# Kernel optimization log

Measured on AMD Instinct MI355X. Metric: run time of the kernel, lower is better.

## Reference

```python
import jax, jax.numpy as jnp
import numpy as np
from math import sqrt

D_MODEL, D_COND, N_HEADS = 512, 768, 8
B, H, W, L_COND = 8, 64, 64, 256


def setup_inputs() -> dict:
    key = jax.random.key(0)
    ks = jax.random.split(key, 7)
    return {
        "image": jax.random.normal(ks[0], (B, D_MODEL, H, W), jnp.float32),
        "cond": jax.random.normal(ks[1], (B, L_COND, D_COND), jnp.float32),
        "attention_mask": jnp.zeros((B, H * W, L_COND), jnp.float32),
        "Wq": jax.random.normal(ks[2], (D_MODEL, D_MODEL), jnp.float32) * 0.02,
        "Wk": jax.random.normal(ks[3], (D_MODEL, D_COND), jnp.float32) * 0.02,
        "Wv": jax.random.normal(ks[4], (D_MODEL, D_COND), jnp.float32) * 0.02,
        "Wo": jax.random.normal(ks[5], (D_MODEL, D_MODEL), jnp.float32) * 0.02,
        "bo": jnp.zeros((D_MODEL,), jnp.float32),
    }


def reference(image, cond, attention_mask, Wq, Wk, Wv, Wo, bo):
    b, d, h, w = image.shape
    L = h * w
    n = N_HEADS
    dh = d // n
    scale = sqrt(dh)
    # b d h w -> b l d
    x = image.reshape(b, d, L).transpose(0, 2, 1)
    # projections (torch Linear: y = x @ W.T), split heads: b l (n dh) -> b n l dh
    q = (x @ Wq.T).reshape(b, L, n, dh).transpose(0, 2, 1, 3)
    k = (cond @ Wk.T).reshape(b, -1, n, dh).transpose(0, 2, 1, 3)
    v = (cond @ Wv.T).reshape(b, -1, n, dh).transpose(0, 2, 1, 3)
    attn = jnp.einsum("bnqd,bnkd->bnqk", q, k) / scale
    attn = attn + attention_mask[:, None]  # b 1 L L_cond
    p = jax.nn.softmax(attn, axis=-1)
    o = jnp.einsum("bnqk,bnkd->bnqd", p, v)  # b n L dh
    # b n (h w) dh -> b (n dh) h w
    o = o.transpose(0, 1, 3, 2).reshape(b, d, h, w)
    # 1x1 conv == per-pixel linear over channels
    out = jnp.einsum("oc,bchw->bohw", Wo, o) + bo[None, :, None, None]
    return out
```

## Files before the change

### kernel.cpp

```cpp
#include <hip/hip_runtime.h>

typedef __bf16 bf16x8 __attribute__((ext_vector_type(8)));
typedef float f32x4 __attribute__((ext_vector_type(4)));
typedef short s4 __attribute__((ext_vector_type(4)));
typedef unsigned short ush;

#define DEV __device__ __forceinline__


DEV ush f2bf(float x){
  union { float f; unsigned u; } v; v.f = x;
  unsigned r = v.u + 0x7FFFu + ((v.u >> 16) & 1u);
  return (ush)(r >> 16);
}

DEV short bfcast(float x){
  union { __bf16 h; short s; } cv; cv.h = (__bf16)x; return cv.s;
}

DEV void gload_lds16(const ush* g, ush* l){
  __builtin_amdgcn_global_load_lds(
      (const __attribute__((address_space(1))) unsigned int*)g,
      (__attribute__((address_space(3))) unsigned int*)l, 16, 0, 0);
}

__global__ __launch_bounds__(256) void tc_kernel(const float* __restrict__ img, ush* __restrict__ xT){
  __shared__ float tile[32][33];
  const int b = blockIdx.z;
  const int l0 = blockIdx.x << 5, c0 = blockIdx.y << 5;
  const int tx = threadIdx.x & 31, ty = threadIdx.x >> 5;
  const float* src = img + ((size_t)b*512 + c0)*4096 + l0;
  #pragma unroll
  for (int i = 0; i < 32; i += 8) tile[ty+i][tx] = src[(size_t)(ty+i)*4096 + tx];
  __syncthreads();
  ush* dst = xT + ((size_t)b*4096 + l0)*512 + c0;
  #pragma unroll
  for (int i = 0; i < 32; i += 8) dst[(size_t)(ty+i)*512 + tx] = f2bf(tile[tx][ty+i]);
}

__global__ __launch_bounds__(256) void cvt_kernel(const float* c0,const float* c1,const float* c2,
                                                  const float* c3,const float* c4,
                                                  ush* o0, ush* o1, ush* o2, ush* o3, ush* o4){
  const int N0=1572864, N1=262144, N2=393216, N3=393216, N4=262144;
  const int stride = gridDim.x * blockDim.x;
  for (int i = blockIdx.x*blockDim.x + threadIdx.x; i < N0+N1+N2+N3+N4; i += stride){
    int j = i; const float* s; ush* d;
    if (j < N0){ s=c0; d=o0; }
    else { j-=N0; if (j<N1){s=c1;d=o1;}
      else { j-=N1; if (j<N2){s=c2;d=o2;}
        else { j-=N2; if (j<N3){s=c3;d=o3;} else { j-=N3; s=c4; d=o4; } } } }
    d[j] = f2bf(s[j]);
  }
}

DEV void gemm_core(const ush* __restrict__ Ag, long long a_row0, int lda,
                   const ush* __restrict__ Bg, long long b_row0, int ldb,
                   int K, ush* As, ush* Bs, f32x4 acc[4][4])
{
  const int t = threadIdx.x;
  const int lane = t & 63;
  const int wid = t >> 6, wr = wid >> 1, wc = wid & 1;
  #pragma unroll
  for (int mt=0;mt<4;mt++)
    #pragma unroll
    for (int nt=0;nt<4;nt++) acc[mt][nt] = f32x4{0.f,0.f,0.f,0.f};

  const int nk = K >> 6;
  for (int kt = 0; kt < nk; ++kt){
    const int k0 = kt << 6;
    #pragma unroll
    for (int r = 0; r < 4; ++r){
      int idx = (r<<8) + t;
      int row = idx >> 3, slot = idx & 7;
      gload_lds16(Ag + (a_row0 + row)*(long long)lda + k0 + ((slot ^ (row&7))<<3), As + idx*8);
    }
    #pragma unroll
    for (int r = 0; r < 4; ++r){
      int idx = (r<<8) + t;
      int row = idx >> 3, slot = idx & 7;
      gload_lds16(Bg + (b_row0 + row)*(long long)ldb + k0 + ((slot ^ (row&7))<<3), Bs + idx*8);
    }
    __syncthreads();
    #pragma unroll
    for (int kk = 0; kk < 2; ++kk){
      bf16x8 af[4], bfv[4];
      #pragma unroll
      for (int mt=0;mt<4;mt++){
        int row = (wr<<6) + (mt<<4) + (lane & 15);
        int byte = (row<<7) + (kk<<6) + ((lane>>4)<<4);
        byte ^= (row & 7) << 4;
        af[mt] = *(const bf16x8*)((const char*)As + byte);
      }
      #pragma unroll
      for (int nt=0;nt<4;nt++){
        int row = (wc<<6) + (nt<<4) + (lane & 15);
        int byte = (row<<7) + (kk<<6) + ((lane>>4)<<4);
        byte ^= (row & 7) << 4;
        bfv[nt] = *(const bf16x8*)((const char*)Bs + byte);
      }
      #pragma unroll
      for (int mt=0;mt<4;mt++)
        #pragma unroll
        for (int nt=0;nt<4;nt++)
          acc[mt][nt] = __builtin_amdgcn_mfma_f32_16x16x32_bf16(af[mt], bfv[nt], acc[mt][nt], 0,0,0);
    }
    __syncthreads();
  }
}

__global__ __launch_bounds__(256,2) void qproj_kernel(const ush* __restrict__ xT, const ush* __restrict__ Wqb,
                                                      ush* __restrict__ Qg){
  __shared__ ush As[8192], Bs[8192];
  f32x4 acc[4][4];
  const int mb = blockIdx.x & 255, nb = blockIdx.x >> 8;
  gemm_core(xT, (long long)mb*128, 512, Wqb, (long long)nb*128, 512, 512, As, Bs, acc);
  const int lane = threadIdx.x & 63, wid = threadIdx.x >> 6, wr = wid>>1, wc = wid&1;
  #pragma unroll
  for (int mt=0;mt<4;mt++)
    #pragma unroll
    for (int nt=0;nt<4;nt++)
      #pragma unroll
      for (int r=0;r<4;r++){
        int m = mb*128 + (wr<<6) + (mt<<4) + ((lane>>4)<<2) + r;
        int n = (nb<<7) + (wc<<6) + (nt<<4) + (lane&15);
        int bb = m >> 12, l = m & 4095, hh = n >> 6, dh = n & 63;
        Qg[(((size_t)(bb*8 + hh)*4096 + l)<<6) + dh] = f2bf(acc[mt][nt][r] * 0.180336880f);
      }
}

__global__ __launch_bounds__(256,2) void kvproj_kernel(const ush* __restrict__ cb, const ush* __restrict__ Wkb,
                                                       const ush* __restrict__ Wvb, ush* __restrict__ Kg,
                                                       ush* __restrict__ Vt){
  __shared__ ush As[8192], Bs[8192];
  f32x4 acc[4][4];
  const int which = blockIdx.z;
  const int nb = blockIdx.x & 3, mb = blockIdx.x >> 2;
  gemm_core(cb, (long long)mb*128, 768, which ? Wvb : Wkb, (long long)nb*128, 768, 768, As, Bs, acc);
  const int lane = threadIdx.x & 63, wid = threadIdx.x >> 6, wr = wid>>1, wc = wid&1;
  #pragma unroll
  for (int mt=0;mt<4;mt++)
    #pragma unroll
    for (int nt=0;nt<4;nt++)
      #pragma unroll
      for (int r=0;r<4;r++){
        int m = mb*128 + (wr<<6) + (mt<<4) + ((lane>>4)<<2) + r;
        int n = (nb<<7) + (wc<<6) + (nt<<4) + (lane&15);
        int bb = m >> 8, j = m & 255;
        ush val = f2bf(acc[mt][nt][r]);
        if (!which) Kg[(((size_t)(bb*256 + j))<<9) + n] = val;
        else { int hh = n>>6, dh = n&63; Vt[(((size_t)((bb*8+hh)*64 + dh))<<8) + j] = val; }
      }
}

__global__ __launch_bounds__(512,2) void attn_kernel(const ush* __restrict__ Qg, const ush* __restrict__ Kg,
                                                     const ush* __restrict__ Vg, const float* __restrict__ mask,
                                                     ush* __restrict__ Oc){
  extern __shared__ char smem[];
  ush* Ks = (ush*)smem;
  ush* Vs = (ush*)(smem + 32768);
  const int t = threadIdx.x, lane = t & 63, wid = t >> 6;
  const int qb = blockIdx.x, h = blockIdx.y, b = blockIdx.z;
  const float L2E = 1.44269504f;

  #pragma unroll
  for (int r = 0; r < 4; ++r){
    int idx = (r<<9) + t;
    int j = idx >> 3, slot = idx & 7;
    gload_lds16(Kg + ((size_t)(b*256 + j))*512 + h*64 + ((slot ^ (j&7))<<3), Ks + idx*8);
  }
  #pragma unroll
  for (int r = 0; r < 4; ++r){
    int idx = (r<<9) + t;
    int dh = idx >> 5, slot = idx & 31;
    gload_lds16(Vg + ((size_t)((b*8 + h)*64 + dh))*256 + ((((slot&7) ^ (dh&7)) | (slot&24))<<3), Vs + idx*8);
  }
  __syncthreads();

  const int l15 = lane & 15, kg = lane >> 4;
  const ush* Qbase = Qg + ((size_t)(b*8 + h)*4096)*64;
  const int q00 = qb*512 + wid*64;

  #pragma unroll 1
  for (int mp = 0; mp < 2; ++mp){
    const int qA = q00 + mp*32 + l15;
    const int qB = qA + 16;
    bf16x8 qf00 = *(const bf16x8*)(Qbase + (size_t)qA*64 + (kg<<3));
    bf16x8 qf01 = *(const bf16x8*)(Qbase + (size_t)qA*64 + 32 + (kg<<3));
    bf16x8 qf10 = *(const bf16x8*)(Qbase + (size_t)qB*64 + (kg<<3));
    bf16x8 qf11 = *(const bf16x8*)(Qbase + (size_t)qB*64 + 32 + (kg<<3));
    const float* mrowA = mask + ((size_t)b*4096 + qA)*256 + (kg<<2);
    const float* mrowB = mrowA + (16<<8);

    f32x4 oaccA[4], oaccB[4];
    #pragma unroll
    for (int tl=0;tl<4;++tl){ oaccA[tl] = f32x4{0.f,0.f,0.f,0.f}; oaccB[tl] = f32x4{0.f,0.f,0.f,0.f}; }
    float mA = 0.f, mB = 0.f;
    f32x4 svA = f32x4{0.f,0.f,0.f,0.f}, svB = f32x4{0.f,0.f,0.f,0.f};

    #pragma unroll 1
    for (int qt = 0; qt < 4; ++qt){
      f32x4 sA[4], sB[4];
      #pragma unroll
      for (int nt=0;nt<4;++nt){ sA[nt] = f32x4{0.f,0.f,0.f,0.f}; sB[nt] = f32x4{0.f,0.f,0.f,0.f}; }
      #pragma unroll
      for (int nt=0;nt<4;++nt){
        int row = (qt<<6) + (nt<<4) + l15;
        const char* kb = (const char*)Ks + (row<<7);
        int sw = (row&7)<<4;
        bf16x8 kf0 = *(const bf16x8*)(kb + ((kg<<4) ^ sw));
        bf16x8 kf1 = *(const bf16x8*)(kb + (((kg<<4)+64) ^ sw));
        sA[nt] = __builtin_amdgcn_mfma_f32_16x16x32_bf16(kf0, qf00, sA[nt], 0,0,0);
        sA[nt] = __builtin_amdgcn_mfma_f32_16x16x32_bf16(kf1, qf01, sA[nt], 0,0,0);
        sB[nt] = __builtin_amdgcn_mfma_f32_16x16x32_bf16(kf0, qf10, sB[nt], 0,0,0);
        sB[nt] = __builtin_amdgcn_mfma_f32_16x16x32_bf16(kf1, qf11, sB[nt], 0,0,0);
      }

      float mxA = -3.0e38f, mxB = -3.0e38f;
      #pragma unroll
      for (int nt=0;nt<4;++nt){
        float4 va = *(const float4*)(mrowA + (qt<<6) + (nt<<4));
        float4 vb = *(const float4*)(mrowB + (qt<<6) + (nt<<4));
        sA[nt][0] = fmaf(va.x, L2E, sA[nt][0]); sA[nt][1] = fmaf(va.y, L2E, sA[nt][1]);
        sA[nt][2] = fmaf(va.z, L2E, sA[nt][2]); sA[nt][3] = fmaf(va.w, L2E, sA[nt][3]);
        sB[nt][0] = fmaf(vb.x, L2E, sB[nt][0]); sB[nt][1] = fmaf(vb.y, L2E, sB[nt][1]);
        sB[nt][2] = fmaf(vb.z, L2E, sB[nt][2]); sB[nt][3] = fmaf(vb.w, L2E, sB[nt][3]);
        #pragma unroll
        for (int r=0;r<4;++r){ mxA = fmaxf(mxA, sA[nt][r]); mxB = fmaxf(mxB, sB[nt][r]); }
      }
      mxA = fmaxf(mxA, __shfl_xor(mxA, 16, 64));
      mxA = fmaxf(mxA, __shfl_xor(mxA, 32, 64));
      mxB = fmaxf(mxB, __shfl_xor(mxB, 16, 64));
      mxB = fmaxf(mxB, __shfl_xor(mxB, 32, 64));

      if (qt == 0){
        mA = mxA; mB = mxB;
      } else if (!__all(fmaxf(mxA - mA, mxB - mB) <= 8.f)){
        float mnA = fmaxf(mA, mxA), mnB = fmaxf(mB, mxB);
        float aA = exp2f(mA - mnA), aB = exp2f(mB - mnB);
        #pragma unroll
        for (int r=0;r<4;++r){ svA[r] *= aA; svB[r] *= aB; }
        #pragma unroll
        for (int tl=0;tl<4;++tl)
          #pragma unroll
          for (int r=0;r<4;++r){ oaccA[tl][r] *= aA; oaccB[tl][r] *= aB; }
        mA = mnA; mB = mnB;
      }

      #pragma unroll
      for (int nt=0;nt<4;++nt){
        s4 pA, pB;
        #pragma unroll
        for (int r=0;r<4;++r){
          float pa = exp2f(sA[nt][r] - mA);
          float pb = exp2f(sB[nt][r] - mB);
          svA[r] += pa; svB[r] += pb;
          pA[r] = bfcast(pa); pB[r] = bfcast(pb);
        }
        #pragma unroll
        for (int tl=0;tl<4;++tl){
          int dr = (tl<<4) + l15;
          int off = ((qt<<7) + (nt<<5) + (kg<<3)) ^ ((dr&7)<<4);
          s4 vf = *(const s4*)((const char*)Vs + (dr<<9) + off);
          oaccA[tl] = __builtin_amdgcn_mfma_f32_16x16x16bf16_1k(vf, pA, oaccA[tl], 0,0,0);
          oaccB[tl] = __builtin_amdgcn_mfma_f32_16x16x16bf16_1k(vf, pB, oaccB[tl], 0,0,0);
        }
      }
      __builtin_amdgcn_sched_barrier(0);
    }

    float sAt = (svA[0]+svA[1]) + (svA[2]+svA[3]);
    float sBt = (svB[0]+svB[1]) + (svB[2]+svB[3]);
    sAt += __shfl_xor(sAt, 16, 64); sAt += __shfl_xor(sAt, 32, 64);
    sBt += __shfl_xor(sBt, 16, 64); sBt += __shfl_xor(sBt, 32, 64);
    const float rlA = 1.f / sAt, rlB = 1.f / sBt;
    #pragma unroll
    for (int tl=0;tl<4;++tl){
      s4 ovA, ovB;
      #pragma unroll
      for (int r=0;r<4;++r){ ovA[r] = bfcast(oaccA[tl][r] * rlA); ovB[r] = bfcast(oaccB[tl][r] * rlB); }
      *(s4*)(Oc + (((size_t)b*4096 + qA)<<9) + h*64 + (tl<<4) + (kg<<2)) = ovA;
      *(s4*)(Oc + (((size_t)b*4096 + qB)<<9) + h*64 + (tl<<4) + (kg<<2)) = ovB;
    }
  }
}

__global__ __launch_bounds__(256,2) void oproj_kernel(const ush* __restrict__ Wob, const ush* __restrict__ Oc,
                                                      const float* __restrict__ bo, float* __restrict__ out){
  __shared__ ush As[8192], Bs[8192];
  f32x4 acc[4][4];
  const int bz = blockIdx.z;
  const int mb = blockIdx.x >> 5, nb = blockIdx.x & 31;
  gemm_core(Wob, (long long)mb*128, 512, Oc + (size_t)bz*4096*512, (long long)nb*128, 512, 512, As, Bs, acc);
  const int lane = threadIdx.x & 63, wid = threadIdx.x >> 6, wr = wid>>1, wc = wid&1;
  #pragma unroll
  for (int mt=0;mt<4;mt++)
    #pragma unroll
    for (int nt=0;nt<4;nt++){
      #pragma unroll
      for (int r=0;r<4;r++){
        int m = (mb<<7) + (wr<<6) + (mt<<4) + ((lane>>4)<<2) + r;
        int n = (nb<<7) + (wc<<6) + (nt<<4) + (lane&15);
        out[(((size_t)(bz*512 + m))<<12) + n] = acc[mt][nt][r] + bo[m];
      }
    }
}

extern "C" void kernel_launch(void* const* d_in, const int* in_sizes, int n_in,
                              void* d_out, int out_size, void* d_ws, size_t ws_size,
                              hipStream_t stream){
  const float* image = (const float*)d_in[0];
  const float* cond  = (const float*)d_in[1];
  const float* mask  = (const float*)d_in[2];
  const float* Wq    = (const float*)d_in[3];
  const float* Wk    = (const float*)d_in[4];
  const float* Wv    = (const float*)d_in[5];
  const float* Wo    = (const float*)d_in[6];
  const float* bo    = (const float*)d_in[7];
  float* out = (float*)d_out;

  char* ws = (char*)d_ws;
  ush* xT   = (ush*)(ws);
  ush* Oc   = xT;
  ush* Qg   = (ush*)(ws + 33554432);
  ush* cndb = (ush*)(ws + 67108864);
  ush* Kg   = (ush*)(ws + 70254592);
  ush* Vt   = (ush*)(ws + 72351744);
  ush* Wqb  = (ush*)(ws + 74448896);
  ush* Wkb  = (ush*)(ws + 74973184);
  ush* Wvb  = (ush*)(ws + 75759616);
  ush* Wob  = (ush*)(ws + 76546048);

  (void)hipFuncSetAttribute((const void*)attn_kernel,
                            hipFuncAttributeMaxDynamicSharedMemorySize, 65536);

  tc_kernel<<<dim3(128,16,8), 256, 0, stream>>>(image, xT);
  cvt_kernel<<<dim3(1024), 256, 0, stream>>>(cond, Wq, Wk, Wv, Wo, cndb, Wqb, Wkb, Wvb, Wob);
  qproj_kernel<<<dim3(1024), 256, 0, stream>>>(xT, Wqb, Qg);
  kvproj_kernel<<<dim3(64,1,2), 256, 0, stream>>>(cndb, Wkb, Wvb, Kg, Vt);
  attn_kernel<<<dim3(8,8,8), 512, 65536, stream>>>(Qg, Kg, Vt, mask, Oc);
  oproj_kernel<<<dim3(128,1,8), 256, 0, stream>>>(Wob, Oc, bo, out);
}
```

Measured before the change: 160.1 us.

## Read K/V directly from global memory in attention, drop LDS staging

The attention kernel no longer stages per-head K and V tiles into 64KB of LDS. Each wave now reads its MFMA fragments straight from global memory (expected to be served from L2/cache) and handles one 32-row query pair. The grid grows to four times as many 256-thread blocks, one pass per block. This removes the LDS fill, the barrier and the LDS occupancy limit, but adds redundant, poorly coalesced global loads of K and V across waves and blocks.

```diff
diff --git a/kernel.cpp b/kernel.cpp
--- a/kernel.cpp
+++ b/kernel.cpp
@@ -152,135 +152,114 @@
       }
 }
 
-__global__ __launch_bounds__(512,2) void attn_kernel(const ush* __restrict__ Qg, const ush* __restrict__ Kg,
-                                                     const ush* __restrict__ Vg, const float* __restrict__ mask,
-                                                     ush* __restrict__ Oc){
-  extern __shared__ char smem[];
-  ush* Ks = (ush*)smem;
-  ush* Vs = (ush*)(smem + 32768);
+__global__ __launch_bounds__(256) void attn_kernel(const ush* __restrict__ Qg, const ush* __restrict__ Kg,
+                                                   const ush* __restrict__ Vg, const float* __restrict__ mask,
+                                                   ush* __restrict__ Oc){
   const int t = threadIdx.x, lane = t & 63, wid = t >> 6;
   const int qb = blockIdx.x, h = blockIdx.y, b = blockIdx.z;
   const float L2E = 1.44269504f;
-
-  #pragma unroll
-  for (int r = 0; r < 4; ++r){
-    int idx = (r<<9) + t;
-    int j = idx >> 3, slot = idx & 7;
-    gload_lds16(Kg + ((size_t)(b*256 + j))*512 + h*64 + ((slot ^ (j&7))<<3), Ks + idx*8);
+  const int l15 = lane & 15, kg = lane >> 4;
+
+  const ush* Kb = Kg + ((size_t)b*256)*512 + h*64;
+  const ush* Vb = Vg + ((size_t)(b*8 + h)*64)*256;
+  const ush* Qbase = Qg + ((size_t)(b*8 + h)*4096)*64;
+
+  const int qA = qb*128 + wid*32 + l15;
+  const int qB = qA + 16;
+  bf16x8 qf00 = *(const bf16x8*)(Qbase + (size_t)qA*64 + (kg<<3));
+  bf16x8 qf01 = *(const bf16x8*)(Qbase + (size_t)qA*64 + 32 + (kg<<3));
+  bf16x8 qf10 = *(const bf16x8*)(Qbase + (size_t)qB*64 + (kg<<3));
+  bf16x8 qf11 = *(const bf16x8*)(Qbase + (size_t)qB*64 + 32 + (kg<<3));
+  const float* mrowA = mask + ((size_t)b*4096 + qA)*256 + (kg<<2);
+  const float* mrowB = mrowA + (16<<8);
+
+  f32x4 oaccA[4], oaccB[4];
+  #pragma unroll
+  for (int tl=0;tl<4;++tl){ oaccA[tl] = f32x4{0.f,0.f,0.f,0.f}; oaccB[tl] = f32x4{0.f,0.f,0.f,0.f}; }
+  float mA = 0.f, mB = 0.f;
+  f32x4 svA = f32x4{0.f,0.f,0.f,0.f}, svB = f32x4{0.f,0.f,0.f,0.f};
+
+  #pragma unroll 1
+  for (int qt = 0; qt < 4; ++qt){
+    f32x4 sA[4], sB[4];
+    #pragma unroll
+    for (int nt=0;nt<4;++nt){ sA[nt] = f32x4{0.f,0.f,0.f,0.f}; sB[nt] = f32x4{0.f,0.f,0.f,0.f}; }
+    #pragma unroll
+    for (int nt=0;nt<4;++nt){
+      int row = (qt<<6) + (nt<<4) + l15;
+      const ush* kr = Kb + (size_t)row*512 + (kg<<3);
+      bf16x8 kf0 = *(const bf16x8*)(kr);
+      bf16x8 kf1 = *(const bf16x8*)(kr + 32);
+      sA[nt] = __builtin_amdgcn_mfma_f32_16x16x32_bf16(kf0, qf00, sA[nt], 0,0,0);
+      sA[nt] = __builtin_amdgcn_mfma_f32_16x16x32_bf16(kf1, qf01, sA[nt], 0,0,0);
+      sB[nt] = __builtin_amdgcn_mfma_f32_16x16x32_bf16(kf0, qf10, sB[nt], 0,0,0);
+      sB[nt] = __builtin_amdgcn_mfma_f32_16x16x32_bf16(kf1, qf11, sB[nt], 0,0,0);
+    }
+
+    float mxA = -3.0e38f, mxB = -3.0e38f;
+    #pragma unroll
+    for (int nt=0;nt<4;++nt){
+      float4 va = *(const float4*)(mrowA + (qt<<6) + (nt<<4));
+      float4 vb = *(const float4*)(mrowB + (qt<<6) + (nt<<4));
+      sA[nt][0] = fmaf(va.x, L2E, sA[nt][0]); sA[nt][1] = fmaf(va.y, L2E, sA[nt][1]);
+      sA[nt][2] = fmaf(va.z, L2E, sA[nt][2]); sA[nt][3] = fmaf(va.w, L2E, sA[nt][3]);
+      sB[nt][0] = fmaf(vb.x, L2E, sB[nt][0]); sB[nt][1] = fmaf(vb.y, L2E, sB[nt][1]);
+      sB[nt][2] = fmaf(vb.z, L2E, sB[nt][2]); sB[nt][3] = fmaf(vb.w, L2E, sB[nt][3]);
+      #pragma unroll
+      for (int r=0;r<4;++r){ mxA = fmaxf(mxA, sA[nt][r]); mxB = fmaxf(mxB, sB[nt][r]); }
+    }
+    mxA = fmaxf(mxA, __shfl_xor(mxA, 16, 64));
+    mxA = fmaxf(mxA, __shfl_xor(mxA, 32, 64));
+    mxB = fmaxf(mxB, __shfl_xor(mxB, 16, 64));
+    mxB = fmaxf(mxB, __shfl_xor(mxB, 32, 64));
+
+    if (qt == 0){
+      mA = mxA; mB = mxB;
+    } else if (!__all(fmaxf(mxA - mA, mxB - mB) <= 8.f)){
+      float mnA = fmaxf(mA, mxA), mnB = fmaxf(mB, mxB);
+      float aA = exp2f(mA - mnA), aB = exp2f(mB - mnB);
+      #pragma unroll
+      for (int r=0;r<4;++r){ svA[r] *= aA; svB[r] *= aB; }
+      #pragma unroll
+      for (int tl=0;tl<4;++tl)
+        #pragma unroll
+        for (int r=0;r<4;++r){ oaccA[tl][r] *= aA; oaccB[tl][r] *= aB; }
+      mA = mnA; mB = mnB;
+    }
+
+    #pragma unroll
+    for (int nt=0;nt<4;++nt){
+      s4 pA, pB;
+      #pragma unroll
+      for (int r=0;r<4;++r){
+        float pa = exp2f(sA[nt][r] - mA);
+        float pb = exp2f(sB[nt][r] - mB);
+        svA[r] += pa; svB[r] += pb;
+        pA[r] = bfcast(pa); pB[r] = bfcast(pb);
+      }
+      #pragma unroll
+      for (int tl=0;tl<4;++tl){
+        int dr = (tl<<4) + l15;
+        s4 vf = *(const s4*)(Vb + (size_t)dr*256 + (qt<<6) + (nt<<4) + (kg<<2));
+        oaccA[tl] = __builtin_amdgcn_mfma_f32_16x16x16bf16_1k(vf, pA, oaccA[tl], 0,0,0);
+        oaccB[tl] = __builtin_amdgcn_mfma_f32_16x16x16bf16_1k(vf, pB, oaccB[tl], 0,0,0);
+      }
+    }
+    __builtin_amdgcn_sched_barrier(0);
   }
-  #pragma unroll
-  for (int r = 0; r < 4; ++r){
-    int idx = (r<<9) + t;
-    int dh = idx >> 5, slot = idx & 31;
-    gload_lds16(Vg + ((size_t)((b*8 + h)*64 + dh))*256 + ((((slot&7) ^ (dh&7)) | (slot&24))<<3), Vs + idx*8);
-  }
-  __syncthreads();
-
-  const int l15 = lane & 15, kg = lane >> 4;
-  const ush* Qbase = Qg + ((size_t)(b*8 + h)*4096)*64;
-  const int q00 = qb*512 + wid*64;
-
-  #pragma unroll 1
-  for (int mp = 0; mp < 2; ++mp){
-    const int qA = q00 + mp*32 + l15;
-    const int qB = qA + 16;
-    bf16x8 qf00 = *(const bf16x8*)(Qbase + (size_t)qA*64 + (kg<<3));
-    bf16x8 qf01 = *(const bf16x8*)(Qbase + (size_t)qA*64 + 32 + (kg<<3));
-    bf16x8 qf10 = *(const bf16x8*)(Qbase + (size_t)qB*64 + (kg<<3));
-    bf16x8 qf11 = *(const bf16x8*)(Qbase + (size_t)qB*64 + 32 + (kg<<3));
-    const float* mrowA = mask + ((size_t)b*4096 + qA)*256 + (kg<<2);
-    const float* mrowB = mrowA + (16<<8);
-
-    f32x4 oaccA[4], oaccB[4];
-    #pragma unroll
-    for (int tl=0;tl<4;++tl){ oaccA[tl] = f32x4{0.f,0.f,0.f,0.f}; oaccB[tl] = f32x4{0.f,0.f,0.f,0.f}; }
-    float mA = 0.f, mB = 0.f;
-    f32x4 svA = f32x4{0.f,0.f,0.f,0.f}, svB = f32x4{0.f,0.f,0.f,0.f};
-
-    #pragma unroll 1
-    for (int qt = 0; qt < 4; ++qt){
-      f32x4 sA[4], sB[4];
-      #pragma unroll
-      for (int nt=0;nt<4;++nt){ sA[nt] = f32x4{0.f,0.f,0.f,0.f}; sB[nt] = f32x4{0.f,0.f,0.f,0.f}; }
-      #pragma unroll
-      for (int nt=0;nt<4;++nt){
-        int row = (qt<<6) + (nt<<4) + l15;
-        const char* kb = (const char*)Ks + (row<<7);
-        int sw = (row&7)<<4;
-        bf16x8 kf0 = *(const bf16x8*)(kb + ((kg<<4) ^ sw));
-        bf16x8 kf1 = *(const bf16x8*)(kb + (((kg<<4)+64) ^ sw));
-        sA[nt] = __builtin_amdgcn_mfma_f32_16x16x32_bf16(kf0, qf00, sA[nt], 0,0,0);
-        sA[nt] = __builtin_amdgcn_mfma_f32_16x16x32_bf16(kf1, qf01, sA[nt], 0,0,0);
-        sB[nt] = __builtin_amdgcn_mfma_f32_16x16x32_bf16(kf0, qf10, sB[nt], 0,0,0);
-        sB[nt] = __builtin_amdgcn_mfma_f32_16x16x32_bf16(kf1, qf11, sB[nt], 0,0,0);
-      }
-
-      float mxA = -3.0e38f, mxB = -3.0e38f;
-      #pragma unroll
-      for (int nt=0;nt<4;++nt){
-        float4 va = *(const float4*)(mrowA + (qt<<6) + (nt<<4));
-        float4 vb = *(const float4*)(mrowB + (qt<<6) + (nt<<4));
-        sA[nt][0] = fmaf(va.x, L2E, sA[nt][0]); sA[nt][1] = fmaf(va.y, L2E, sA[nt][1]);
-        sA[nt][2] = fmaf(va.z, L2E, sA[nt][2]); sA[nt][3] = fmaf(va.w, L2E, sA[nt][3]);
-        sB[nt][0] = fmaf(vb.x, L2E, sB[nt][0]); sB[nt][1] = fmaf(vb.y, L2E, sB[nt][1]);
-        sB[nt][2] = fmaf(vb.z, L2E, sB[nt][2]); sB[nt][3] = fmaf(vb.w, L2E, sB[nt][3]);
-        #pragma unroll
-        for (int r=0;r<4;++r){ mxA = fmaxf(mxA, sA[nt][r]); mxB = fmaxf(mxB, sB[nt][r]); }
-      }
-      mxA = fmaxf(mxA, __shfl_xor(mxA, 16, 64));
-      mxA = fmaxf(mxA, __shfl_xor(mxA, 32, 64));
-      mxB = fmaxf(mxB, __shfl_xor(mxB, 16, 64));
-      mxB = fmaxf(mxB, __shfl_xor(mxB, 32, 64));
-
-      if (qt == 0){
-        mA = mxA; mB = mxB;
-      } else if (!__all(fmaxf(mxA - mA, mxB - mB) <= 8.f)){
-        float mnA = fmaxf(mA, mxA), mnB = fmaxf(mB, mxB);
-        float aA = exp2f(mA - mnA), aB = exp2f(mB - mnB);
-        #pragma unroll
-        for (int r=0;r<4;++r){ svA[r] *= aA; svB[r] *= aB; }
-        #pragma unroll
-        for (int tl=0;tl<4;++tl)
-          #pragma unroll
-          for (int r=0;r<4;++r){ oaccA[tl][r] *= aA; oaccB[tl][r] *= aB; }
-        mA = mnA; mB = mnB;
-      }
-
-      #pragma unroll
-      for (int nt=0;nt<4;++nt){
-        s4 pA, pB;
-        #pragma unroll
-        for (int r=0;r<4;++r){
-          float pa = exp2f(sA[nt][r] - mA);
-          float pb = exp2f(sB[nt][r] - mB);
-          svA[r] += pa; svB[r] += pb;
-          pA[r] = bfcast(pa); pB[r] = bfcast(pb);
-        }
-        #pragma unroll
-        for (int tl=0;tl<4;++tl){
-          int dr = (tl<<4) + l15;
-          int off = ((qt<<7) + (nt<<5) + (kg<<3)) ^ ((dr&7)<<4);
-          s4 vf = *(const s4*)((const char*)Vs + (dr<<9) + off);
-          oaccA[tl] = __builtin_amdgcn_mfma_f32_16x16x16bf16_1k(vf, pA, oaccA[tl], 0,0,0);
-          oaccB[tl] = __builtin_amdgcn_mfma_f32_16x16x16bf16_1k(vf, pB, oaccB[tl], 0,0,0);
-        }
-      }
-      __builtin_amdgcn_sched_barrier(0);
-    }
-
-    float sAt = (svA[0]+svA[1]) + (svA[2]+svA[3]);
-    float sBt = (svB[0]+svB[1]) + (svB[2]+svB[3]);
-    sAt += __shfl_xor(sAt, 16, 64); sAt += __shfl_xor(sAt, 32, 64);
-    sBt += __shfl_xor(sBt, 16, 64); sBt += __shfl_xor(sBt, 32, 64);
-    const float rlA = 1.f / sAt, rlB = 1.f / sBt;
-    #pragma unroll
-    for (int tl=0;tl<4;++tl){
-      s4 ovA, ovB;
-      #pragma unroll
-      for (int r=0;r<4;++r){ ovA[r] = bfcast(oaccA[tl][r] * rlA); ovB[r] = bfcast(oaccB[tl][r] * rlB); }
-      *(s4*)(Oc + (((size_t)b*4096 + qA)<<9) + h*64 + (tl<<4) + (kg<<2)) = ovA;
-      *(s4*)(Oc + (((size_t)b*4096 + qB)<<9) + h*64 + (tl<<4) + (kg<<2)) = ovB;
-    }
+
+  float sAt = (svA[0]+svA[1]) + (svA[2]+svA[3]);
+  float sBt = (svB[0]+svB[1]) + (svB[2]+svB[3]);
+  sAt += __shfl_xor(sAt, 16, 64); sAt += __shfl_xor(sAt, 32, 64);
+  sBt += __shfl_xor(sBt, 16, 64); sBt += __shfl_xor(sBt, 32, 64);
+  const float rlA = 1.f / sAt, rlB = 1.f / sBt;
+  #pragma unroll
+  for (int tl=0;tl<4;++tl){
+    s4 ovA, ovB;
+    #pragma unroll
+    for (int r=0;r<4;++r){ ovA[r] = bfcast(oaccA[tl][r] * rlA); ovB[r] = bfcast(oaccB[tl][r] * rlB); }
+    *(s4*)(Oc + (((size_t)b*4096 + qA)<<9) + h*64 + (tl<<4) + (kg<<2)) = ovA;
+    *(s4*)(Oc + (((size_t)b*4096 + qB)<<9) + h*64 + (tl<<4) + (kg<<2)) = ovB;
   }
 }
 
@@ -330,13 +309,10 @@
   ush* Wvb  = (ush*)(ws + 75759616);
   ush* Wob  = (ush*)(ws + 76546048);
 
-  (void)hipFuncSetAttribute((const void*)attn_kernel,
-                            hipFuncAttributeMaxDynamicSharedMemorySize, 65536);
-
   tc_kernel<<<dim3(128,16,8), 256, 0, stream>>>(image, xT);
   cvt_kernel<<<dim3(1024), 256, 0, stream>>>(cond, Wq, Wk, Wv, Wo, cndb, Wqb, Wkb, Wvb, Wob);
   qproj_kernel<<<dim3(1024), 256, 0, stream>>>(xT, Wqb, Qg);
   kvproj_kernel<<<dim3(64,1,2), 256, 0, stream>>>(cndb, Wkb, Wvb, Kg, Vt);
-  attn_kernel<<<dim3(8,8,8), 512, 65536, stream>>>(Qg, Kg, Vt, mask, Oc);
+  attn_kernel<<<dim3(32,8,8), 256, 0, stream>>>(Qg, Kg, Vt, mask, Oc);
   oproj_kernel<<<dim3(128,1,8), 256, 0, stream>>>(Wob, Oc, bo, out);
 }
```

New measurement: 231.2 us. 44.4% more time.
